# Kernel optimization log

Measured on AMD Instinct MI355X. Metric: run time of the kernel, lower is better.

Reference implementation:

```python
import jax, jax.numpy as jnp
import numpy as np

MAX_SCALE = 10  # matches init_kwargs max_scale


def setup_inputs() -> dict:
    key = jax.random.key(0)
    # [B, H, W, D, C] as consumed by keras MaxPooling3D (channels_last)
    x = jax.random.normal(key, (8, 224, 224, 8, 8), dtype=jnp.float32)
    return {"x": x}


def reference(x):
    # For each scale s in 1..MAX_SCALE: max-pool over (H, W) with an s x s
    # window, stride 1, VALID padding (pool dim 3 has window 1), then sum the
    # pooled map over the two pooled spatial axes -> [B, D, C].
    boxes_at_scale = []
    for scale in range(1, MAX_SCALE + 1):
        pooled = jax.lax.reduce_window(
            x,
            -jnp.inf,
            jax.lax.max,
            window_dimensions=(1, scale, scale, 1, 1),
            window_strides=(1, 1, 1, 1, 1),
            padding="VALID",
        )  # [B, H-s+1, W-s+1, D, C]
        boxes_at_scale.append(jnp.sum(pooled, axis=(1, 2)))  # [B, D, C]
    stacked = jnp.stack(boxes_at_scale, axis=-1)  # [B, D, C, MAX_SCALE]
    return jax.nn.relu(stacked) + 1.0
```

## Files before the change

kernel.cpp:

```cpp
#include <hip/hip_runtime.h>

#define BB 8
#define HH 224
#define WW 224
#define DCH 64
#define NS 10
#define SEG 55
#define NSEG 5
#define STRIP 56
#define NHS 4
#define NCG 8
#define NBLK (BB * NCG * NSEG * NHS)

__global__ void zero_kernel(float* out, int n) {
    int i = blockIdx.x * blockDim.x + threadIdx.x;
    if (i < n) out[i] = 0.0f;
}

__global__ void finalize_kernel(float* out, int n) {
    int i = blockIdx.x * blockDim.x + threadIdx.x;
    if (i < n) out[i] = fmaxf(out[i], 0.0f) + 1.0f;
}

__device__ __forceinline__ float dpp_shl1(float v) {
    return __int_as_float(__builtin_amdgcn_update_dpp(
        0, __float_as_int(v), 0x130, 0xF, 0xF, true));
}

template<int PHASE>
__device__ __forceinline__ void row_body(int h, int row0, const float (&m)[NS],
                                         float (&cp)[2], float (&prev)[NS - 1][2],
                                         float (&acc)[NS][2]) {
    if (PHASE != 2) {
        acc[0][0] = fmaf(cp[0], m[0], acc[0][0]);
        acc[0][1] = fmaf(cp[1], m[0], acc[0][1]);
    }
#pragma unroll
    for (int lv = 0; lv < NS - 1; ++lv) {
        float vm0 = fmaxf(prev[lv][0], cp[0]);
        float vm1 = fmaxf(prev[lv][1], cp[1]);
        prev[lv][0] = cp[0];
        prev[lv][1] = cp[1];
        cp[0] = fmaxf(vm0, dpp_shl1(vm0));
        cp[1] = fmaxf(vm1, dpp_shl1(vm1));
        bool on = true;
        if (PHASE == 0) on = (h - lv - 1) >= row0;
        if (PHASE == 2) on = (h - lv - 1) < row0 + STRIP;
        if (on) {
            acc[lv + 1][0] = fmaf(cp[0], m[lv + 1], acc[lv + 1][0]);
            acc[lv + 1][1] = fmaf(cp[1], m[lv + 1], acc[lv + 1][1]);
        }
    }
}

__global__ __launch_bounds__(256, 4) void pool_kernel(const float* __restrict__ x,
                                                      float* __restrict__ out) {
    const int phys = blockIdx.x;
    const int logical = (phys & 7) * (NBLK / 8) + (phys >> 3);
    const int b = logical / (NCG * NSEG * NHS);
    const int r = logical % (NCG * NSEG * NHS);
    const int cg = r & 7;
    const int ws = (r >> 3) % NSEG;
    const int hs = (r >> 3) / NSEG;

    const int wv   = threadIdx.x >> 6;
    const int lane = threadIdx.x & 63;
    const int ch   = cg * 8 + wv * 2;
    const int col  = ws * SEG + lane;
    const int row0 = hs * STRIP;
    const int rend = min(row0 + STRIP + NS - 1, HH);

    float m[NS];
#pragma unroll
    for (int s = 1; s <= NS; ++s)
        m[s - 1] = (lane < SEG && col <= WW - s) ? 1.0f : 0.0f;

    float prev[NS - 1][2], acc[NS][2], cp[2], nv[2];
#pragma unroll
    for (int lv = 0; lv < NS - 1; ++lv) { prev[lv][0] = 0.0f; prev[lv][1] = 0.0f; }
#pragma unroll
    for (int s = 0; s < NS; ++s) { acc[s][0] = 0.0f; acc[s][1] = 0.0f; }
    nv[0] = 0.0f; nv[1] = 0.0f;

    const bool colok = (col < WW);
    const float* px = x + (((size_t)(b * HH + row0) * WW + col) * DCH + ch);
    const ptrdiff_t rstride = (ptrdiff_t)WW * DCH;

    if (colok) { float2 t = *(const float2*)px; nv[0] = t.x; nv[1] = t.y; }

#define ROW_STEP(P)                                                          \
    {                                                                        \
        cp[0] = nv[0]; cp[1] = nv[1];                                        \
        if (h + 1 < rend) {   \
            px += rstride;                                                   \
            if (colok) { float2 t = *(const float2*)px; nv[0] = t.x; nv[1] = t.y; } \
        }                                                                    \
        row_body<P>(h, row0, m, cp, prev, acc);                              \
    }

    int h = row0;
    const int warm_end = row0 + NS - 1;
    for (; h < warm_end; ++h) ROW_STEP(0)
    const int steady_end = min(row0 + STRIP, rend);
    for (; h < steady_end; ++h) ROW_STEP(1)
    for (; h < rend; ++h) ROW_STEP(2)
#undef ROW_STEP

#pragma unroll
    for (int s = 0; s < NS; ++s) {
#pragma unroll
        for (int c = 0; c < 2; ++c) {
            float v = acc[s][c];
#pragma unroll
            for (int off = 32; off > 0; off >>= 1) v += __shfl_xor(v, off);
            if (lane == 0) atomicAdd(&out[((size_t)b * DCH + ch + c) * NS + s], v);
        }
    }
}

extern "C" void kernel_launch(void* const* d_in, const int* in_sizes, int n_in,
                              void* d_out, int out_size, void* d_ws, size_t ws_size,
                              hipStream_t stream) {
    const float* x = (const float*)d_in[0];
    float* out = (float*)d_out;
    const int nblk = (out_size + 255) / 256;
    zero_kernel<<<nblk, 256, 0, stream>>>(out, out_size);
    pool_kernel<<<NBLK, 256, 0, stream>>>(x, out);
    finalize_kernel<<<nblk, 256, 0, stream>>>(out, out_size);
}
```

Measured before the change: 204.7 us.

## Process rows in groups of four with double-buffered prefetch and static boundary masks

Restructures the row loop so that four rows are handled per step. The next four rows are prefetched into an alternate register buffer while the current group is computed, and the max-pyramid work for the four rows is interleaved to expose ILP across the DPP shifts. Warm-up and tail masking move to compile-time group indices, loads are clamped instead of predicted, and the launch-bounds occupancy hint rises from 4 to 5. This costs more registers and code size, and a fixed unroll schedule that depends on the strip length.

```diff
diff --git a/kernel.cpp b/kernel.cpp
--- a/kernel.cpp
+++ b/kernel.cpp
@@ -11,6 +11,7 @@
 #define NHS 4
 #define NCG 8
 #define NBLK (BB * NCG * NSEG * NHS)
+#define RST (WW * DCH)
 
 __global__ void zero_kernel(float* out, int n) {
     int i = blockIdx.x * blockDim.x + threadIdx.x;
@@ -23,42 +24,101 @@
 }
 
 __device__ __forceinline__ float dpp_shl1(float v) {
-    return __int_as_float(__builtin_amdgcn_update_dpp(
-        0, __float_as_int(v), 0x130, 0xF, 0xF, true));
+#if defined(__has_builtin) && __has_builtin(__builtin_amdgcn_mov_dpp)
+    return __int_as_float(__builtin_amdgcn_mov_dpp(__float_as_int(v), 0x130, 0xF, 0xF, true));
+#else
+    return __int_as_float(__builtin_amdgcn_update_dpp(0, __float_as_int(v), 0x130, 0xF, 0xF, true));
+#endif
 }
 
-template<int PHASE>
-__device__ __forceinline__ void row_body(int h, int row0, const float (&m)[NS],
-                                         float (&cp)[2], float (&prev)[NS - 1][2],
-                                         float (&acc)[NS][2]) {
-    if (PHASE != 2) {
-        acc[0][0] = fmaf(cp[0], m[0], acc[0][0]);
-        acc[0][1] = fmaf(cp[1], m[0], acc[0][1]);
-    }
+template<int G>
+__device__ __forceinline__ void group4(float (&c)[4][2], float (&p)[NS - 1][2],
+                                       float (&acc)[NS][2], const float (&m)[NS]) {
+#pragma unroll
+    for (int i = 0; i < 4; ++i)
+        if (G < 0 || 4 * G + i <= 55) {
+#pragma unroll
+            for (int ch = 0; ch < 2; ++ch)
+                acc[0][ch] = fmaf(c[i][ch], m[0], acc[0][ch]);
+        }
 #pragma unroll
     for (int lv = 0; lv < NS - 1; ++lv) {
-        float vm0 = fmaxf(prev[lv][0], cp[0]);
-        float vm1 = fmaxf(prev[lv][1], cp[1]);
-        prev[lv][0] = cp[0];
-        prev[lv][1] = cp[1];
-        cp[0] = fmaxf(vm0, dpp_shl1(vm0));
-        cp[1] = fmaxf(vm1, dpp_shl1(vm1));
-        bool on = true;
-        if (PHASE == 0) on = (h - lv - 1) >= row0;
-        if (PHASE == 2) on = (h - lv - 1) < row0 + STRIP;
-        if (on) {
-            acc[lv + 1][0] = fmaf(cp[0], m[lv + 1], acc[lv + 1][0]);
-            acc[lv + 1][1] = fmaf(cp[1], m[lv + 1], acc[lv + 1][1]);
+        float t[4][2];
+#pragma unroll
+        for (int ch = 0; ch < 2; ++ch) {
+            t[0][ch] = fmaxf(p[lv][ch], c[0][ch]);
+            t[1][ch] = fmaxf(c[0][ch], c[1][ch]);
+            t[2][ch] = fmaxf(c[1][ch], c[2][ch]);
+            t[3][ch] = fmaxf(c[2][ch], c[3][ch]);
+            p[lv][ch] = c[3][ch];
         }
+#pragma unroll
+        for (int i = 0; i < 4; ++i)
+#pragma unroll
+            for (int ch = 0; ch < 2; ++ch)
+                c[i][ch] = fmaxf(t[i][ch], dpp_shl1(t[i][ch]));
+#pragma unroll
+        for (int i = 0; i < 4; ++i)
+            if (G < 0 || (4 * G + i >= lv + 1 && 4 * G + i <= 56 + lv)) {
+#pragma unroll
+                for (int ch = 0; ch < 2; ++ch)
+                    acc[lv + 1][ch] = fmaf(c[i][ch], m[lv + 1], acc[lv + 1][ch]);
+            }
     }
 }
 
-__global__ __launch_bounds__(256, 4) void pool_kernel(const float* __restrict__ x,
+__device__ __forceinline__ void run(const float* __restrict__ px0, int R,
+                                    float (&acc)[NS][2], const float (&m)[NS]) {
+    const int Rm1 = R - 1;
+    float p[NS - 1][2];
+#pragma unroll
+    for (int lv = 0; lv < NS - 1; ++lv) { p[lv][0] = 0.0f; p[lv][1] = 0.0f; }
+    float cvA[4][2], cvB[4][2];
+
+#define PRE4(buf, rb)                                                      \
+    {                                                                      \
+        _Pragma("unroll") for (int i = 0; i < 4; ++i) {                    \
+            const int rr = min((rb) + i, Rm1);                             \
+            const float2 t2 = *(const float2*)(px0 + (size_t)rr * RST);    \
+            buf[i][0] = t2.x; buf[i][1] = t2.y;                            \
+        }                                                                  \
+    }
+
+    PRE4(cvA, 0)
+    PRE4(cvB, 4)  group4<0>(cvA, p, acc, m);
+    PRE4(cvA, 8)  group4<1>(cvB, p, acc, m);
+    PRE4(cvB, 12) group4<2>(cvA, p, acc, m);
+    PRE4(cvA, 16) group4<-1>(cvB, p, acc, m);
+    for (int k = 4; k <= 12; k += 2) {
+        PRE4(cvB, 4 * k + 4) group4<-1>(cvA, p, acc, m);
+        PRE4(cvA, 4 * k + 8) group4<-1>(cvB, p, acc, m);
+    }
+    if (R == STRIP + NS - 1) {
+        PRE4(cvB, 60) group4<14>(cvA, p, acc, m);
+        float last[2];
+        { const float2 t2 = *(const float2*)(px0 + (size_t)(STRIP + 8) * RST);
+          last[0] = t2.x; last[1] = t2.y; }
+        group4<15>(cvB, p, acc, m);
+#pragma unroll
+        for (int lv = 0; lv < NS - 1; ++lv)
+#pragma unroll
+            for (int ch = 0; ch < 2; ++ch) {
+                float t = fmaxf(p[lv][ch], last[ch]);
+                last[ch] = fmaxf(t, dpp_shl1(t));
+            }
+#pragma unroll
+        for (int ch = 0; ch < 2; ++ch)
+            acc[NS - 1][ch] = fmaf(last[ch], m[NS - 1], acc[NS - 1][ch]);
+    }
+#undef PRE4
+}
+
+__global__ __launch_bounds__(256, 5) void pool_kernel(const float* __restrict__ x,
                                                       float* __restrict__ out) {
     const int phys = blockIdx.x;
     const int logical = (phys & 7) * (NBLK / 8) + (phys >> 3);
-    const int b = logical / (NCG * NSEG * NHS);
-    const int r = logical % (NCG * NSEG * NHS);
+    const int b  = logical / (NCG * NSEG * NHS);
+    const int r  = logical % (NCG * NSEG * NHS);
     const int cg = r & 7;
     const int ws = (r >> 3) % NSEG;
     const int hs = (r >> 3) / NSEG;
@@ -68,46 +128,24 @@
     const int ch   = cg * 8 + wv * 2;
     const int col  = ws * SEG + lane;
     const int row0 = hs * STRIP;
-    const int rend = min(row0 + STRIP + NS - 1, HH);
+    const int R    = min(STRIP + NS - 1, HH - row0);
+
+    float acc[NS][2];
+#pragma unroll
+    for (int s = 0; s < NS; ++s) { acc[s][0] = 0.0f; acc[s][1] = 0.0f; }
 
     float m[NS];
 #pragma unroll
     for (int s = 1; s <= NS; ++s)
         m[s - 1] = (lane < SEG && col <= WW - s) ? 1.0f : 0.0f;
 
-    float prev[NS - 1][2], acc[NS][2], cp[2], nv[2];
-#pragma unroll
-    for (int lv = 0; lv < NS - 1; ++lv) { prev[lv][0] = 0.0f; prev[lv][1] = 0.0f; }
-#pragma unroll
-    for (int s = 0; s < NS; ++s) { acc[s][0] = 0.0f; acc[s][1] = 0.0f; }
-    nv[0] = 0.0f; nv[1] = 0.0f;
+    const int colc = min(col, WW - 1);
+    const float* px0 = x + ((size_t)(b * HH + row0) * WW + colc) * DCH + ch;
 
-    const bool colok = (col < WW);
-    const float* px = x + (((size_t)(b * HH + row0) * WW + col) * DCH + ch);
-    const ptrdiff_t rstride = (ptrdiff_t)WW * DCH;
-
-    if (colok) { float2 t = *(const float2*)px; nv[0] = t.x; nv[1] = t.y; }
-
-#define ROW_STEP(P)                                                          \
-    {                                                                        \
-        cp[0] = nv[0]; cp[1] = nv[1];                                        \
-        if (h + 1 < rend) {   \
-            px += rstride;                                                   \
-            if (colok) { float2 t = *(const float2*)px; nv[0] = t.x; nv[1] = t.y; } \
-        }                                                                    \
-        row_body<P>(h, row0, m, cp, prev, acc);                              \
-    }
-
-    int h = row0;
-    const int warm_end = row0 + NS - 1;
-    for (; h < warm_end; ++h) ROW_STEP(0)
-    const int steady_end = min(row0 + STRIP, rend);
-    for (; h < steady_end; ++h) ROW_STEP(1)
-    for (; h < rend; ++h) ROW_STEP(2)
-#undef ROW_STEP
+    run(px0, R, acc, m);
 
 #pragma unroll
-    for (int s = 0; s < NS; ++s) {
+    for (int s = 0; s < NS; ++s)
 #pragma unroll
         for (int c = 0; c < 2; ++c) {
             float v = acc[s][c];
@@ -115,7 +153,6 @@
             for (int off = 32; off > 0; off >>= 1) v += __shfl_xor(v, off);
             if (lane == 0) atomicAdd(&out[((size_t)b * DCH + ch + c) * NS + s], v);
         }
-    }
 }
 
 extern "C" void kernel_launch(void* const* d_in, const int* in_sizes, int n_in,
```

Result: slower. 248.1 us (+21.2%).

## Halve row strips, double-buffer row loads, and fully unroll warmup/tail phases

Applied to the files above, without the earlier changes.

Splits H into 8 strips of 28 rows instead of 4 of 56, which doubles the block count and raises the launch-bounds occupancy hint to 6. Row loads are prefetched two rows ahead, and column addresses are clamped so the per-row branch on valid columns goes away. The warmup and tail phases are unrolled at compile time so their per-level guards become constants, and the DPP move uses mov_dpp. The cost is more redundant halo rows, since each strip reads 9 extra rows, plus more atomics and register pressure.

```diff
diff --git a/kernel.cpp b/kernel.cpp
--- a/kernel.cpp
+++ b/kernel.cpp
@@ -7,10 +7,11 @@
 #define NS 10
 #define SEG 55
 #define NSEG 5
-#define STRIP 56
-#define NHS 4
+#define STRIP 28
+#define NHS 8
 #define NCG 8
 #define NBLK (BB * NCG * NSEG * NHS)
+#define RST (WW * DCH)
 
 __global__ void zero_kernel(float* out, int n) {
     int i = blockIdx.x * blockDim.x + threadIdx.x;
@@ -23,15 +24,13 @@
 }
 
 __device__ __forceinline__ float dpp_shl1(float v) {
-    return __int_as_float(__builtin_amdgcn_update_dpp(
-        0, __float_as_int(v), 0x130, 0xF, 0xF, true));
+    return __int_as_float(__builtin_amdgcn_mov_dpp(__float_as_int(v), 0x130, 0xF, 0xF, true));
 }
 
-template<int PHASE>
-__device__ __forceinline__ void row_body(int h, int row0, const float (&m)[NS],
-                                         float (&cp)[2], float (&prev)[NS - 1][2],
-                                         float (&acc)[NS][2]) {
-    if (PHASE != 2) {
+template<int WI, int TI>
+__device__ __forceinline__ void row_body(const float (&m)[NS], float (&cp)[2],
+                                         float (&prev)[NS - 1][2], float (&acc)[NS][2]) {
+    if (TI < 0) {
         acc[0][0] = fmaf(cp[0], m[0], acc[0][0]);
         acc[0][1] = fmaf(cp[1], m[0], acc[0][1]);
     }
@@ -44,8 +43,8 @@
         cp[0] = fmaxf(vm0, dpp_shl1(vm0));
         cp[1] = fmaxf(vm1, dpp_shl1(vm1));
         bool on = true;
-        if (PHASE == 0) on = (h - lv - 1) >= row0;
-        if (PHASE == 2) on = (h - lv - 1) < row0 + STRIP;
+        if (WI >= 0) on = (WI >= lv + 1);
+        if (TI >= 0) on = (lv >= TI);
         if (on) {
             acc[lv + 1][0] = fmaf(cp[0], m[lv + 1], acc[lv + 1][0]);
             acc[lv + 1][1] = fmaf(cp[1], m[lv + 1], acc[lv + 1][1]);
@@ -53,12 +52,12 @@
     }
 }
 
-__global__ __launch_bounds__(256, 4) void pool_kernel(const float* __restrict__ x,
+__global__ __launch_bounds__(256, 6) void pool_kernel(const float* __restrict__ x,
                                                       float* __restrict__ out) {
     const int phys = blockIdx.x;
     const int logical = (phys & 7) * (NBLK / 8) + (phys >> 3);
-    const int b = logical / (NCG * NSEG * NHS);
-    const int r = logical % (NCG * NSEG * NHS);
+    const int b  = logical / (NCG * NSEG * NHS);
+    const int r  = logical % (NCG * NSEG * NHS);
     const int cg = r & 7;
     const int ws = (r >> 3) % NSEG;
     const int hs = (r >> 3) / NSEG;
@@ -68,46 +67,65 @@
     const int ch   = cg * 8 + wv * 2;
     const int col  = ws * SEG + lane;
     const int row0 = hs * STRIP;
-    const int rend = min(row0 + STRIP + NS - 1, HH);
+    const int R    = min(STRIP + NS - 1, HH - row0);
 
     float m[NS];
 #pragma unroll
     for (int s = 1; s <= NS; ++s)
         m[s - 1] = (lane < SEG && col <= WW - s) ? 1.0f : 0.0f;
 
-    float prev[NS - 1][2], acc[NS][2], cp[2], nv[2];
+    float prev[NS - 1][2], acc[NS][2], cp[2], n1[2], n2[2];
 #pragma unroll
     for (int lv = 0; lv < NS - 1; ++lv) { prev[lv][0] = 0.0f; prev[lv][1] = 0.0f; }
 #pragma unroll
     for (int s = 0; s < NS; ++s) { acc[s][0] = 0.0f; acc[s][1] = 0.0f; }
-    nv[0] = 0.0f; nv[1] = 0.0f;
 
-    const bool colok = (col < WW);
-    const float* px = x + (((size_t)(b * HH + row0) * WW + col) * DCH + ch);
-    const ptrdiff_t rstride = (ptrdiff_t)WW * DCH;
+    const int colc = min(col, WW - 1);
+    const float* px0 = x + ((size_t)(b * HH + row0) * WW + colc) * DCH + ch;
 
-    if (colok) { float2 t = *(const float2*)px; nv[0] = t.x; nv[1] = t.y; }
+    { const float2 t = *(const float2*)px0;                    n1[0] = t.x; n1[1] = t.y; }
+    { const float2 t = *(const float2*)(px0 + (size_t)RST);    n2[0] = t.x; n2[1] = t.y; }
 
-#define ROW_STEP(P)                                                          \
+#define WSTEP(i)                                                             \
     {                                                                        \
-        cp[0] = nv[0]; cp[1] = nv[1];                                        \
-        if (h + 1 < rend) {   \
-            px += rstride;                                                   \
-            if (colok) { float2 t = *(const float2*)px; nv[0] = t.x; nv[1] = t.y; } \
-        }                                                                    \
-        row_body<P>(h, row0, m, cp, prev, acc);                              \
+        cp[0] = n1[0]; cp[1] = n1[1]; n1[0] = n2[0]; n1[1] = n2[1];          \
+        const float2 t2 = *(const float2*)(px0 + (size_t)((i) + 2) * RST);   \
+        n2[0] = t2.x; n2[1] = t2.y;                                          \
+        row_body<(i), -1>(m, cp, prev, acc);                                 \
+    }
+    WSTEP(0) WSTEP(1) WSTEP(2) WSTEP(3) WSTEP(4)
+    WSTEP(5) WSTEP(6) WSTEP(7) WSTEP(8)
+#undef WSTEP
+
+    {
+        const int rel_end = min(STRIP, R);
+#pragma unroll 2
+        for (int rel = NS - 1; rel < rel_end; ++rel) {
+            cp[0] = n1[0]; cp[1] = n1[1]; n1[0] = n2[0]; n1[1] = n2[1];
+            const int rr = min(rel + 2, R - 1);
+            const float2 t2 = *(const float2*)(px0 + (size_t)rr * RST);
+            n2[0] = t2.x; n2[1] = t2.y;
+            row_body<-1, -1>(m, cp, prev, acc);
+        }
     }
 
-    int h = row0;
-    const int warm_end = row0 + NS - 1;
-    for (; h < warm_end; ++h) ROW_STEP(0)
-    const int steady_end = min(row0 + STRIP, rend);
-    for (; h < steady_end; ++h) ROW_STEP(1)
-    for (; h < rend; ++h) ROW_STEP(2)
-#undef ROW_STEP
+    if (R == STRIP + NS - 1) {
+#define TSTEP(i)                                                             \
+    {                                                                        \
+        cp[0] = n1[0]; cp[1] = n1[1]; n1[0] = n2[0]; n1[1] = n2[1];          \
+        const int rr = ((i) + STRIP + 2 < STRIP + NS - 1) ? (i) + STRIP + 2  \
+                                                          : STRIP + NS - 2;  \
+        const float2 t2 = *(const float2*)(px0 + (size_t)rr * RST);          \
+        n2[0] = t2.x; n2[1] = t2.y;                                          \
+        row_body<-1, (i)>(m, cp, prev, acc);                                 \
+    }
+        TSTEP(0) TSTEP(1) TSTEP(2) TSTEP(3) TSTEP(4)
+        TSTEP(5) TSTEP(6) TSTEP(7) TSTEP(8)
+#undef TSTEP
+    }
 
 #pragma unroll
-    for (int s = 0; s < NS; ++s) {
+    for (int s = 0; s < NS; ++s)
 #pragma unroll
         for (int c = 0; c < 2; ++c) {
             float v = acc[s][c];
@@ -115,7 +133,6 @@
             for (int off = 32; off > 0; off >>= 1) v += __shfl_xor(v, off);
             if (lane == 0) atomicAdd(&out[((size_t)b * DCH + ch + c) * NS + s], v);
         }
-    }
 }
 
 extern "C" void kernel_launch(void* const* d_in, const int* in_sizes, int n_in,
```

Result: slower. 268.8 us (+31.3%).
